# Performance work log

Hardware: AMD Instinct MI355X
Metric: run time of the kernel (lower is better)

## Reference

```python
import math
import jax, jax.numpy as jnp
import numpy as np

BLOCK = 32          # hard-coded in the CUDA kernels
NUM_HEADS = 16
NUM_BLOCKS = 512    # (max_pos//32) * block_per_row = 128 * 4
DIAG_N = 3
FIRST_N = 0


def _mra2_attention(Q, K, V, mask):
    # Q,K,V: (meta_batch, seq, head_dim); mask: (meta_batch, seq) in {0,1}
    mb, seq_len, d = Q.shape
    bs = BLOCK
    nb = seq_len // bs
    scale = 1.0 / math.sqrt(d)
    Q = Q * mask[:, :, None]
    K = K * mask[:, :, None]
    V = V * mask[:, :, None]

    # ---- low resolution block means (mask-weighted), approx_mode='full' keeps V_hat
    tc = mask.reshape(mb, nb, bs).sum(-1)                 # token count per block
    denom = tc[:, :, None] + 1e-6
    Q_hat = Q.reshape(mb, nb, bs, d).sum(2) / denom       # (mb, nb, d)
    K_hat = K.reshape(mb, nb, bs, d).sum(2) / denom
    V_hat = V.reshape(mb, nb, bs, d).sum(2) / denom
    low_logit = jnp.einsum('bid,bjd->bij', Q_hat, K_hat) * scale
    row_max = low_logit.max(-1, keepdims=True)            # before mask subtraction
    low_logit = low_logit - 10000.0 * ((tc[:, None, :] * tc[:, :, None]) < 0.5).astype(Q.dtype)

    # ---- block index selection (torch runs this under no_grad)
    lrn = jax.lax.stop_gradient(low_logit - row_max)
    if DIAG_N > 0:
        off = DIAG_N // 2
        i = jnp.arange(nb)
        band = (jnp.abs(i[:, None] - i[None, :]) <= off).astype(Q.dtype)
        lrn = lrn + band[None] * 5000.0
    if FIRST_N > 0:
        lrn = lrn.at[:, :FIRST_N, :].add(5000.0)
        lrn = lrn.at[:, :, :FIRST_N].add(5000.0)
    top_vals, indices = jax.lax.top_k(lrn.reshape(mb, nb * nb), NUM_BLOCKS)
    threshold = top_vals.min(-1)
    high_mask = (lrn >= threshold[:, None, None]).astype(Q.dtype)  # selected-block mask

    q_blk = indices // nb                                  # (mb, n) query block ids
    k_blk = indices % nb                                   # (mb, n) key block ids
    Qs = jnp.take_along_axis(Q.reshape(mb, nb, bs, d), q_blk[:, :, None, None], axis=1)
    Ks = jnp.take_along_axis(K.reshape(mb, nb, bs, d), k_blk[:, :, None, None], axis=1)
    Vs = jnp.take_along_axis(V.reshape(mb, nb, bs, d), k_blk[:, :, None, None], axis=1)

    # sampled dense-dense: sparse_C[b,n,k,q] (key-in-block, query-in-block layout as in kernel)
    hi_logit = jnp.einsum('bnkd,bnqd->bnkq', Ks, Qs) * scale

    # per query-row max over selected blocks (kernel index_max; constant for grad)
    b_idx = jnp.arange(mb)[:, None]
    blk_max = hi_logit.max(axis=2)                         # (mb, n, bs) max over key axis
    max_blocks = jnp.full((mb, nb, bs), -1e8, Q.dtype).at[b_idx, q_blk].max(blk_max)
    max_blocks = jax.lax.stop_gradient(max_blocks)
    max_vals = max_blocks.reshape(mb, seq_len)
    max_scatter = jnp.take_along_axis(max_blocks, q_blk[:, :, None], axis=1)[:, :, None, :]

    # key-side mask per selected block (sparse_mask_B)
    mask_blk = jnp.take_along_axis(mask.reshape(mb, nb, bs), k_blk[:, :, None], axis=1)
    hi_attn = jnp.exp(hi_logit - max_scatter - 10000.0 * (1.0 - mask_blk[:, :, :, None]))

    # sparse-dense matmul + reduce-sum normalizer, scattered back per query block
    hi_out = jnp.zeros((mb, nb, bs, d), Q.dtype).at[b_idx, q_blk].add(
        jnp.einsum('bnkq,bnkd->bnqd', hi_attn, Vs)).reshape(mb, seq_len, d)
    hi_norm = jnp.zeros((mb, nb, bs), Q.dtype).at[b_idx, q_blk].add(
        hi_attn.sum(axis=2)).reshape(mb, seq_len)

    # ---- low resolution branch, selected blocks suppressed via high_mask
    low_attn = jnp.exp(low_logit - row_max - 10000.0 * high_mask) * tc[:, None, :]
    low_out = jnp.repeat(jnp.einsum('bij,bjd->bid', low_attn, V_hat), bs, axis=1)
    low_norm = jnp.repeat(low_attn.sum(-1), bs, axis=1)

    log_corr = (jnp.repeat(row_max[:, :, 0], bs, axis=1) - max_vals) * mask
    low_corr = jnp.exp(jnp.minimum(log_corr, 0.0))
    hi_corr = jnp.exp(-jnp.maximum(log_corr, 0.0))

    ctx = hi_out * hi_corr[:, :, None] + low_out * low_corr[:, :, None]
    ctx = ctx / (hi_norm * hi_corr + low_norm * low_corr + 1e-6)[:, :, None]
    return ctx * mask[:, :, None]


def _forward(hidden_states, attention_mask, w_q, b_q, w_k, b_k, w_v, b_v):
    b, s, hdim = hidden_states.shape
    h = NUM_HEADS
    dh = hdim // h

    def split_heads(x):
        return x.reshape(b, s, h, dh).transpose(0, 2, 1, 3).reshape(b * h, s, dh)

    q = split_heads(hidden_states @ w_q.T + b_q)
    k = split_heads(hidden_states @ w_k.T + b_k)
    v = split_heads(hidden_states @ w_v.T + b_v)
    # invert extended additive mask (1 + am/10000) and replicate over heads
    # (torch's .repeat(1, h, 1).reshape(b*h, s) stacks h copies of the [b,s] mask)
    mask = jnp.tile(1.0 + attention_mask / 10000.0, (h, 1))
    ctx = _mra2_attention(q, k, v, mask)
    ctx = ctx.reshape(b, h, s, dh).transpose(0, 2, 1, 3).reshape(b, s, hdim)
    return ctx


def setup_inputs() -> dict:
    key = jax.random.key(0)
    ks = jax.random.split(key, 4)
    H = 1024
    return {
        'hidden_states': jax.random.normal(ks[0], (2, 4096, H), jnp.float32),
        'attention_mask': jnp.zeros((2, 4096), jnp.float32),
        'w_q': jax.random.normal(ks[1], (H, H), jnp.float32) * 0.02,
        'b_q': jnp.zeros((H,), jnp.float32),
        'w_k': jax.random.normal(ks[2], (H, H), jnp.float32) * 0.02,
        'b_k': jnp.zeros((H,), jnp.float32),
        'w_v': jax.random.normal(ks[3], (H, H), jnp.float32) * 0.02,
        'b_v': jnp.zeros((H,), jnp.float32),
    }


def reference(hidden_states, attention_mask, w_q, b_q, w_k, b_k, w_v, b_v):
    return _forward(hidden_states, attention_mask, w_q, b_q, w_k, b_k, w_v, b_v)
```

## Files before the change

kernel.cpp:

```cpp
#include <hip/hip_runtime.h>
#include <cstdint>
#include <cstddef>

#define MAXSEL 160
static constexpr int S    = 4096;
static constexpr int H    = 1024;
static constexpr int DH   = 64;
static constexpr int NB   = 128;
static constexpr int MBH  = 32;
static constexpr int M8   = 8192;
static constexpr int N3   = 3072;

typedef _Float16 half8 __attribute__((ext_vector_type(8)));
typedef _Float16 half4v __attribute__((ext_vector_type(4)));
typedef float floatx4 __attribute__((ext_vector_type(4)));

__device__ __forceinline__ void load_lds16(const void* g, void* l) {
  __builtin_amdgcn_global_load_lds((const __attribute__((address_space(1))) unsigned int*)g,
                                   (__attribute__((address_space(3))) unsigned int*)l,
                                   16, 0, 0);
}

__global__ __launch_bounds__(256) void k_prep(const float* __restrict__ hidden,
                                              const float* __restrict__ am,
                                              const float* __restrict__ wq,
                                              const float* __restrict__ wk,
                                              const float* __restrict__ wv,
                                              _Float16* __restrict__ h16,
                                              _Float16* __restrict__ w16,
                                              _Float16* __restrict__ wlo,
                                              _Float16* __restrict__ hb_hi,
                                              _Float16* __restrict__ hb_lo,
                                              float* __restrict__ tcv,
                                              int* __restrict__ selcnt) {
  const int blk_id = blockIdx.x;
  if (blk_id < 256) {
    if (blk_id == 0) {
      for (int i = threadIdx.x; i < MBH * NB; i += 256) selcnt[i] = 0;
    }
    int b2 = blk_id >> 7, blk = blk_id & 127;
    int c = threadIdx.x * 4;
    float4 s0 = make_float4(0.f, 0.f, 0.f, 0.f);
    float4 s1 = make_float4(0.f, 0.f, 0.f, 0.f);
    for (int i = 0; i < 32; i += 4) {
      int pos0 = blk * 32 + i;
      size_t base = ((size_t)b2 * 4096 + pos0) * 1024 + c;
      const float4 x0 = *(const float4*)&hidden[base];
      const float4 x1 = *(const float4*)&hidden[base + 1024];
      const float4 x2 = *(const float4*)&hidden[base + 2048];
      const float4 x3 = *(const float4*)&hidden[base + 3072];
      float a00 = am[pos0],      a01 = am[pos0 + 1],      a02 = am[pos0 + 2],      a03 = am[pos0 + 3];
      float a10 = am[4096+pos0], a11 = am[4096+pos0 + 1], a12 = am[4096+pos0 + 2], a13 = am[4096+pos0 + 3];
      half4v h;
      h[0]=(_Float16)x0.x; h[1]=(_Float16)x0.y; h[2]=(_Float16)x0.z; h[3]=(_Float16)x0.w;
      *(half4v*)&h16[base] = h;
      h[0]=(_Float16)x1.x; h[1]=(_Float16)x1.y; h[2]=(_Float16)x1.z; h[3]=(_Float16)x1.w;
      *(half4v*)&h16[base + 1024] = h;
      h[0]=(_Float16)x2.x; h[1]=(_Float16)x2.y; h[2]=(_Float16)x2.z; h[3]=(_Float16)x2.w;
      *(half4v*)&h16[base + 2048] = h;
      h[0]=(_Float16)x3.x; h[1]=(_Float16)x3.y; h[2]=(_Float16)x3.z; h[3]=(_Float16)x3.w;
      *(half4v*)&h16[base + 3072] = h;
      float m0, m1;
      m0 = 1.f + a00 * 1e-4f; m1 = 1.f + a10 * 1e-4f;
      s0.x += m0*x0.x; s0.y += m0*x0.y; s0.z += m0*x0.z; s0.w += m0*x0.w;
      s1.x += m1*x0.x; s1.y += m1*x0.y; s1.z += m1*x0.z; s1.w += m1*x0.w;
      m0 = 1.f + a01 * 1e-4f; m1 = 1.f + a11 * 1e-4f;
      s0.x += m0*x1.x; s0.y += m0*x1.y; s0.z += m0*x1.z; s0.w += m0*x1.w;
      s1.x += m1*x1.x; s1.y += m1*x1.y; s1.z += m1*x1.z; s1.w += m1*x1.w;
      m0 = 1.f + a02 * 1e-4f; m1 = 1.f + a12 * 1e-4f;
      s0.x += m0*x2.x; s0.y += m0*x2.y; s0.z += m0*x2.z; s0.w += m0*x2.w;
      s1.x += m1*x2.x; s1.y += m1*x2.y; s1.z += m1*x2.z; s1.w += m1*x2.w;
      m0 = 1.f + a03 * 1e-4f; m1 = 1.f + a13 * 1e-4f;
      s0.x += m0*x3.x; s0.y += m0*x3.y; s0.z += m0*x3.z; s0.w += m0*x3.w;
      s1.x += m1*x3.x; s1.y += m1*x3.y; s1.z += m1*x3.z; s1.w += m1*x3.w;
    }
    size_t row0 = (size_t)(b2 * 2 + 0) * 128 + blk;
    size_t row1 = (size_t)(b2 * 2 + 1) * 128 + blk;
    half4v hi, lo;
    hi[0]=(_Float16)s0.x; lo[0]=(_Float16)(s0.x-(float)hi[0]);
    hi[1]=(_Float16)s0.y; lo[1]=(_Float16)(s0.y-(float)hi[1]);
    hi[2]=(_Float16)s0.z; lo[2]=(_Float16)(s0.z-(float)hi[2]);
    hi[3]=(_Float16)s0.w; lo[3]=(_Float16)(s0.w-(float)hi[3]);
    *(half4v*)&hb_hi[row0 * 1024 + c] = hi;
    *(half4v*)&hb_lo[row0 * 1024 + c] = lo;
    hi[0]=(_Float16)s1.x; lo[0]=(_Float16)(s1.x-(float)hi[0]);
    hi[1]=(_Float16)s1.y; lo[1]=(_Float16)(s1.y-(float)hi[1]);
    hi[2]=(_Float16)s1.z; lo[2]=(_Float16)(s1.z-(float)hi[2]);
    hi[3]=(_Float16)s1.w; lo[3]=(_Float16)(s1.w-(float)hi[3]);
    *(half4v*)&hb_hi[row1 * 1024 + c] = hi;
    *(half4v*)&hb_lo[row1 * 1024 + c] = lo;
    if (b2 == 0 && threadIdx.x == 0) {
      float t0 = 0.f, t1 = 0.f;
      for (int i = 0; i < 32; ++i) {
        int pos = blk * 32 + i;
        t0 += 1.f + am[pos] * 1e-4f;
        t1 += 1.f + am[4096 + pos] * 1e-4f;
      }
      tcv[blk] = t0; tcv[128 + blk] = t1;
    }
  } else {
    long j = (long)(blk_id - 256) * 256 + threadIdx.x;
    const long NW4 = (long)H * H / 4;
    int which = (int)(j / NW4);
    long jj = j - (long)which * NW4;
    const float* src = which == 0 ? wq : (which == 1 ? wk : wv);
    float4 x = ((const float4*)src)[jj];
    half4v h;
    h[0] = (_Float16)x.x; h[1] = (_Float16)x.y;
    h[2] = (_Float16)x.z; h[3] = (_Float16)x.w;
    *(half4v*)&w16[j * 4] = h;
    if (which < 2) {
      half4v r;
      r[0] = (_Float16)(x.x - (float)h[0]);
      r[1] = (_Float16)(x.y - (float)h[1]);
      r[2] = (_Float16)(x.z - (float)h[2]);
      r[3] = (_Float16)(x.w - (float)h[3]);
      *(half4v*)&wlo[j * 4] = r;
    }
  }
}

__global__ __launch_bounds__(512, 4) void k_gemm_qkv(const _Float16* __restrict__ A,
                                                     const _Float16* __restrict__ B,
                                                     const float* __restrict__ bq,
                                                     const float* __restrict__ bk,
                                                     const float* __restrict__ bv,
                                                     const float* __restrict__ am,
                                                     _Float16* __restrict__ q16,
                                                     _Float16* __restrict__ k16,
                                                     _Float16* __restrict__ v16,
                                                     const _Float16* __restrict__ Ahi,
                                                     const _Float16* __restrict__ Alo,
                                                     const _Float16* __restrict__ Blo,
                                                     float* __restrict__ sideQK) {
  __shared__ _Float16 sh[36864];

  if (blockIdx.x < 768) {
    const int id = blockIdx.x;
    const int swz = (id & 7) * 96 + (id >> 3);
    const int by = swz / 12;
    const int bx = swz - by * 12;
    const int tid = threadIdx.x;
    const int lane = tid & 63, wv = tid >> 6;
    const int wm = wv >> 2, wn = wv & 3;
    const int l15 = lane & 15, quad = lane >> 4;

    _Float16* As = sh;
    _Float16* Bs = sh + 12288;

    floatx4 acc[4][4] = {};

    const _Float16* Ag = A + (size_t)(by * 128) * 1024;
    const _Float16* Bg = B + (size_t)(bx * 256) * 1024;

    const int gr  = lane >> 2;
    const int gcb = ((lane & 3) ^ ((lane >> 3) & 3)) * 8;
    const _Float16* agl  = Ag + (size_t)(wv * 16 + gr) * 1024 + gcb;
    const _Float16* bgl0 = Bg + (size_t)(wv * 32 + gr) * 1024 + gcb;
    const _Float16* bgl1 = Bg + (size_t)(wv * 32 + 16 + gr) * 1024 + gcb;
    const int aw  = (wv * 16) * 32;
    const int bw0 = (wv * 32) * 32;
    const int bw1 = (wv * 32 + 16) * 32;

#define STAGE(TT, BB)                                                   \
    {                                                                   \
      load_lds16(agl  + (size_t)(TT) * 32, &As[(BB) * 4096 + aw]);      \
      load_lds16(bgl0 + (size_t)(TT) * 32, &Bs[(BB) * 8192 + bw0]);     \
      load_lds16(bgl1 + (size_t)(TT) * 32, &Bs[(BB) * 8192 + bw1]);     \
    }

    STAGE(0, 0)
    STAGE(1, 1)

    const int rc = ((quad ^ ((l15 >> 1) & 3)) << 3);

#pragma unroll
    for (int t = 0; t < 32; ++t) {
      if (t == 31) { asm volatile("s_waitcnt vmcnt(0)" ::: "memory"); }
      else         { asm volatile("s_waitcnt vmcnt(3)" ::: "memory"); }
      __builtin_amdgcn_s_barrier();
      if (t < 30) {
        const int nb = (t + 2) % 3;
        STAGE(t + 2, nb)
      }
      const int bb = t % 3;
      half8 a[4], b[4];
#pragma unroll
      for (int mt = 0; mt < 4; ++mt)
        a[mt] = *(const half8*)&As[bb * 4096 + (wm * 64 + mt * 16 + l15) * 32 + rc];
#pragma unroll
      for (int nt = 0; nt < 4; ++nt)
        b[nt] = *(const half8*)&Bs[bb * 8192 + (wn * 64 + nt * 16 + l15) * 32 + rc];
      __builtin_amdgcn_s_setprio(1);
#pragma unroll
      for (int mt = 0; mt < 4; ++mt)
#pragma unroll
        for (int nt = 0; nt < 4; ++nt)
          acc[mt][nt] = __builtin_amdgcn_mfma_f32_16x16x32_f16(a[mt], b[nt], acc[mt][nt], 0, 0, 0);
      __builtin_amdgcn_s_setprio(0);
    }
#undef STAGE

    const int which = bx >> 2;
    const float* bias = which == 0 ? bq : (which == 1 ? bk : bv);
    _Float16* dst = which == 0 ? q16 : (which == 1 ? k16 : v16);
    const int hh = (bx & 3) * 4 + wn;
    const int m2 = hh & 1;
#pragma unroll
    for (int nt = 0; nt < 4; ++nt) {
      const int dd = nt * 16 + l15;
      const float bsv = bias[hh * 64 + dd];
#pragma unroll
      for (int mt = 0; mt < 4; ++mt) {
#pragma unroll
        for (int r = 0; r < 4; ++r) {
          int srow = by * 128 + wm * 64 + mt * 16 + quad * 4 + r;
          int b2 = srow >> 12, s = srow & 4095;
          float mv = 1.f + am[m2 * 4096 + s] * 1e-4f;
          float v = (acc[mt][nt][r] + bsv) * mv;
          int mb = b2 * 16 + hh;
          dst[((size_t)mb * 4096 + s) * 64 + dd] = (_Float16)v;
        }
      }
    }
    return;
  }

  const int half = threadIdx.x >> 8;
  const int stid = threadIdx.x & 255;
  const int sb   = (blockIdx.x - 768) * 2 + half;
  const int slane = stid & 63, swv = stid >> 6;
  const int kk  = sb >> 8;
  const int sbb = sb & 255;
  const int sbx = sbb & 31;
  const int sby = sbb >> 5;
  const int swm = swv >> 1, swn = swv & 1;
  const int sl15 = slane & 15, squad = slane >> 4;
  _Float16* base = sh + half * 16384;
  _Float16* sAhi = base;
  _Float16* sAlo = base + 4096;
  _Float16* sBhi = base + 8192;
  _Float16* sBlo = base + 12288;

  floatx4 acc[2][2] = {};

  const int srow = slane >> 3;
  const int scol = (((slane & 7) ^ (srow & 7)) * 8);
  const int sswz = sl15 & 7;
  const _Float16* src;
  _Float16* dst;
  if      (swv == 0) { src = Ahi + (size_t)(sby * 64) * 1024; dst = sAhi; }
  else if (swv == 1) { src = Alo + (size_t)(sby * 64) * 1024; dst = sAlo; }
  else if (swv == 2) { src = B   + (size_t)(sbx * 64) * 1024; dst = sBhi; }
  else               { src = Blo + (size_t)(sbx * 64) * 1024; dst = sBlo; }

  const int kbeg = kk * 512;
  for (int k0 = kbeg; k0 < kbeg + 512; k0 += 64) {
    __syncthreads();
#pragma unroll
    for (int i = 0; i < 8; ++i)
      load_lds16(src + (size_t)(i * 8 + srow) * 1024 + k0 + scol, dst + i * 512);
    __syncthreads();
#pragma unroll
    for (int ks = 0; ks < 2; ++ks) {
      const int kc = ks * 4;
      half8 ah[2], al[2], bh[2], bl[2];
#pragma unroll
      for (int mt = 0; mt < 2; ++mt) {
        int off = (swm * 32 + mt * 16 + sl15) * 64 + (((kc + squad) ^ sswz) << 3);
        ah[mt] = *(const half8*)&sAhi[off];
        al[mt] = *(const half8*)&sAlo[off];
      }
#pragma unroll
      for (int nt = 0; nt < 2; ++nt) {
        int off = (swn * 32 + nt * 16 + sl15) * 64 + (((kc + squad) ^ sswz) << 3);
        bh[nt] = *(const half8*)&sBhi[off];
        bl[nt] = *(const half8*)&sBlo[off];
      }
#pragma unroll
      for (int mt = 0; mt < 2; ++mt)
#pragma unroll
        for (int nt = 0; nt < 2; ++nt) {
          acc[mt][nt] = __builtin_amdgcn_mfma_f32_16x16x32_f16(ah[mt], bh[nt], acc[mt][nt], 0, 0, 0);
          acc[mt][nt] = __builtin_amdgcn_mfma_f32_16x16x32_f16(ah[mt], bl[nt], acc[mt][nt], 0, 0, 0);
          acc[mt][nt] = __builtin_amdgcn_mfma_f32_16x16x32_f16(al[mt], bh[nt], acc[mt][nt], 0, 0, 0);
        }
    }
  }
  float* outp = sideQK + (size_t)kk * (512 * 2048);
#pragma unroll
  for (int mt = 0; mt < 2; ++mt)
#pragma unroll
    for (int nt = 0; nt < 2; ++nt)
#pragma unroll
      for (int rr = 0; rr < 4; ++rr) {
        int row = sby * 64 + swm * 32 + mt * 16 + squad * 4 + rr;
        int col = sbx * 64 + swn * 32 + nt * 16 + sl15;
        outp[(size_t)row * 2048 + col] = acc[mt][nt][rr];
      }
}

__global__ __launch_bounds__(256) void k_lowlogit(const float* __restrict__ sideQK,
                                                  const float* __restrict__ tcv,
                                                  const float* __restrict__ bq,
                                                  const float* __restrict__ bk,
                                                  float* __restrict__ ll,
                                                  float* __restrict__ rmaxout,
                                                  const _Float16* __restrict__ v16,
                                                  float* __restrict__ vhat,
                                                  _Float16* __restrict__ v16T) {
  __shared__ __attribute__((aligned(16))) char shraw[37376];
  const int tid = threadIdx.x;

  if (blockIdx.x >= 256) {
    const int lane = tid & 63, wv = tid >> 6;
    _Float16* Vs = (_Float16*)shraw + wv * 2304;
    int bid = (blockIdx.x - 256) * 4 + wv;
    int mb = bid >> 7, blk = bid & 127;
    const _Float16* src = v16 + ((size_t)mb * 4096 + blk * 32) * 64;
    int r = lane >> 3, c = (lane & 7) * 8;
#pragma unroll
    for (int it = 0; it < 4; ++it)
      *(uint4*)&Vs[(it * 8 + r) * 72 + c] = *(const uint4*)&src[(it * 8 + r) * 64 + c];
    __syncthreads();
    float acc = 0.f;
    half8 col[4];
#pragma unroll
    for (int k = 0; k < 32; ++k) {
      _Float16 x = Vs[k * 72 + lane];
      col[k >> 3][k & 7] = x;
      acc += (float)x;
    }
    vhat[(size_t)bid * 64 + lane] = acc / (tcv[(mb & 1) * 128 + blk] + 1e-6f);
    _Float16* dst = v16T + (size_t)(mb * 64 + lane) * 4096 + blk * 32;
#pragma unroll
    for (int p = 0; p < 4; ++p) *(half8*)&dst[p * 8] = col[p];
    return;
  }

  const int mb = blockIdx.x >> 3;
  const int ib = blockIdx.x & 7;
  const int b2 = mb >> 4, m2 = mb & 1, hh = mb & 15;
  const int combo = b2 * 2 + m2;
  float* Kh  = (float*)shraw;
  float* Qh  = (float*)(shraw + 32768);
  float* tcL = (float*)(shraw + 32768 + 4096);

  const float* P1 = sideQK + (size_t)512 * 2048;

  if (tid < 128) tcL[tid] = tcv[m2 * 128 + tid];
  __syncthreads();
#pragma unroll
  for (int i = 0; i < 8; ++i) {
    int ci = tid + i * 256;
    int row = ci >> 4, c4 = (ci & 15) * 4;
    float tck = tcL[row];
    float den = 1.f / (tck + 1e-6f);
    size_t idx = ((size_t)combo * 128 + row) * 2048 + 1024 + hh * 64 + c4;
    float4 x0 = *(const float4*)&sideQK[idx];
    float4 x1 = *(const float4*)&P1[idx];
    float4 bb = *(const float4*)&bk[hh * 64 + c4];
    float4 o;
    o.x = (x0.x + x1.x + bb.x * tck) * den; o.y = (x0.y + x1.y + bb.y * tck) * den;
    o.z = (x0.z + x1.z + bb.z * tck) * den; o.w = (x0.w + x1.w + bb.w * tck) * den;
    *(float4*)&Kh[row * 64 + c4] = o;
  }
  {
    int row = tid >> 4, c4 = (tid & 15) * 4;
    int gi = ib * 16 + row;
    float tcq = tcL[gi];
    float den = 1.f / (tcq + 1e-6f);
    size_t idx = ((size_t)combo * 128 + gi) * 2048 + hh * 64 + c4;
    float4 x0 = *(const float4*)&sideQK[idx];
    float4 x1 = *(const float4*)&P1[idx];
    float4 bb = *(const float4*)&bq[hh * 64 + c4];
    float4 o;
    o.x = (x0.x + x1.x + bb.x * tcq) * den; o.y = (x0.y + x1.y + bb.y * tcq) * den;
    o.z = (x0.z + x1.z + bb.z * tcq) * den; o.w = (x0.w + x1.w + bb.w * tcq) * den;
    *(float4*)&Qh[row * 64 + c4] = o;
  }
  __syncthreads();

  const int il = tid >> 4, jg = tid & 15;
  const int i = ib * 16 + il;
  float tcq = tcL[i];
  float dots[8] = {};
#pragma unroll
  for (int dd = 0; dd < 16; ++dd) {
    int d4 = ((dd + tid) & 15) * 4;
    float4 qv = *(const float4*)&Qh[il * 64 + d4];
#pragma unroll
    for (int jj = 0; jj < 8; ++jj) {
      float4 kv = *(const float4*)&Kh[(jg * 8 + jj) * 64 + d4];
      dots[jj] += qv.x * kv.x + qv.y * kv.y + qv.z * kv.z + qv.w * kv.w;
    }
  }
  float tmax = -1e30f;
#pragma unroll
  for (int jj = 0; jj < 8; ++jj) {
    int j = jg * 8 + jj;
    float raw = dots[jj] * 0.125f;
    tmax = fmaxf(tmax, raw);
    float pen = (tcq * tcL[j] < 0.5f) ? 10000.f : 0.f;
    ll[(size_t)mb * 16384 + (size_t)i * 128 + j] = raw - pen;
  }
#pragma unroll
  for (int mk = 1; mk < 16; mk <<= 1) tmax = fmaxf(tmax, __shfl_xor(tmax, mk));
  if (jg == 0) rmaxout[mb * 128 + i] = tmax;
}

__global__ __launch_bounds__(256) void k_topk(const float* __restrict__ ll,
                                              const float* __restrict__ rmax,
                                              float* __restrict__ thr,
                                              int* __restrict__ selcnt,
                                              int* __restrict__ selkb) {
  const int mb = blockIdx.x;
  const int t = threadIdx.x;
  const int wid = t >> 6;
  __shared__ int red2[2][4];

  unsigned code[64];
#pragma unroll
  for (int j = 0; j < 64; ++j) {
    int e = j * 256 + t;
    int i = e >> 7, jj = e & 127;
    float lrn = ll[(size_t)mb * 16384 + e] - rmax[mb * 128 + i];
    int di = i - jj;
    if (di <= 1 && di >= -1) lrn += 5000.f;
    unsigned b = __float_as_uint(lrn);
    code[j] = (b & 0x80000000u) ? ~b : (b | 0x80000000u);
  }

  unsigned lo = 0u, hi = 0xFFFFFFFFu;
  for (int it = 0; it < 32; ++it) {
    unsigned mid = lo + ((hi - lo) >> 1);
    int c = 0;
#pragma unroll
    for (int j = 0; j < 64; ++j) c += (code[j] >= mid) ? 1 : 0;
#pragma unroll
    for (int mk = 1; mk < 64; mk <<= 1) c += __shfl_xor(c, mk);
    if ((t & 63) == 0) red2[it & 1][wid] = c;
    __syncthreads();
    int total = red2[it & 1][0] + red2[it & 1][1] + red2[it & 1][2] + red2[it & 1][3];
    if (total >= 512) lo = mid; else hi = mid;
  }
  if (t == 0) {
    unsigned bits = (lo & 0x80000000u) ? (lo & 0x7FFFFFFFu) : ~lo;
    thr[mb] = __uint_as_float(bits);
  }
#pragma unroll
  for (int j = 0; j < 64; ++j) {
    if (code[j] >= lo) {
      int e = j * 256 + t;
      int i = e >> 7, jj = e & 127;
      int slot = atomicAdd(&selcnt[mb * 128 + i], 1);
      if (slot < MAXSEL) selkb[(size_t)(mb * 128 + i) * MAXSEL + slot] = jj;
    }
  }
}

__global__ __launch_bounds__(64) void k_hi(const _Float16* __restrict__ q16,
                                           const _Float16* __restrict__ k16,
                                           const _Float16* __restrict__ v16T,
                                           const int* __restrict__ selcnt,
                                           const int* __restrict__ selkb,
                                           const float* __restrict__ rmax,
                                           const float* __restrict__ thr,
                                           const float* __restrict__ tcv,
                                           const float* __restrict__ vhat,
                                           const float* __restrict__ ll,
                                           const float* __restrict__ am,
                                           float* __restrict__ out) {
  const int mb = blockIdx.x & 31, qb = blockIdx.x >> 5;
  const int sid = mb * 128 + qb;
  const int lane = threadIdx.x;
  const int l15 = lane & 15, quad = lane >> 4;
  const int m2 = mb & 1, b2 = mb >> 4, hh = mb & 15;

  __shared__ _Float16 Ps[32 * 40];

  const _Float16* qbase = q16 + ((size_t)mb * 4096 + qb * 32) * 64;
  half8 aq[2][2];
#pragma unroll
  for (int mt = 0; mt < 2; ++mt)
#pragma unroll
    for (int ks = 0; ks < 2; ++ks)
      aq[mt][ks] = *(const half8*)&qbase[(mt * 16 + l15) * 64 + ks * 32 + quad * 8];

  const float rmaxb = rmax[sid];
  const float th = thr[mb];
  const float* llrow = ll + (size_t)mb * 16384 + (size_t)qb * 128;
  const float* tcrow = tcv + m2 * 128;
  const float* vhbase = vhat + ((size_t)(mb * 128)) * 64 + lane;
  float a0 = 0.f, a1 = 0.f, a2 = 0.f, a3 = 0.f;
  float n0 = 0.f, n1 = 0.f, n2 = 0.f, n3 = 0.f;
#pragma unroll 2
  for (int j0 = 0; j0 < 128; j0 += 4) {
    float4 l4 = *(const float4*)&llrow[j0];
    float4 t4 = *(const float4*)&tcrow[j0];
    float v0 = vhbase[(size_t)(j0 + 0) * 64];
    float v1 = vhbase[(size_t)(j0 + 1) * 64];
    float v2 = vhbase[(size_t)(j0 + 2) * 64];
    float v3 = vhbase[(size_t)(j0 + 3) * 64];
    int d0 = qb - j0;
    float lr0 = l4.x - rmaxb + ((d0 <= 1 && d0 >= -1) ? 5000.f : 0.f);
    float lr1 = l4.y - rmaxb + ((d0 <= 2 && d0 >= 0) ? 5000.f : 0.f);
    float lr2 = l4.z - rmaxb + ((d0 <= 3 && d0 >= 1) ? 5000.f : 0.f);
    float lr3 = l4.w - rmaxb + ((d0 <= 4 && d0 >= 2) ? 5000.f : 0.f);
    float w0 = (lr0 >= th) ? 0.f : __expf(l4.x - rmaxb) * t4.x;
    float w1 = (lr1 >= th) ? 0.f : __expf(l4.y - rmaxb) * t4.y;
    float w2 = (lr2 >= th) ? 0.f : __expf(l4.z - rmaxb) * t4.z;
    float w3 = (lr3 >= th) ? 0.f : __expf(l4.w - rmaxb) * t4.w;
    a0 += w0 * v0; a1 += w1 * v1; a2 += w2 * v2; a3 += w3 * v3;
    n0 += w0; n1 += w1; n2 += w2; n3 += w3;
  }
  float accL = (a0 + a1) + (a2 + a3);
  float nrmL = (n0 + n1) + (n2 + n3);

  int nk = selcnt[sid];
  if (nk > MAXSEL) nk = MAXSEL;
  const int* list = selkb + (size_t)sid * MAXSEL;

  const _Float16* kbase  = k16  + (size_t)mb * 4096 * 64;
  const _Float16* vtbase = v16T + (size_t)mb * 64 * 4096;

  float rm[2][4];
  floatx4 o[2][4] = {};
  floatx4 onrm[2] = {};
#pragma unroll
  for (int mt = 0; mt < 2; ++mt)
#pragma unroll
    for (int r = 0; r < 4; ++r) rm[mt][r] = -1e8f;

  half8 ones;
#pragma unroll
  for (int j = 0; j < 8; ++j) ones[j] = (_Float16)1.f;

  for (int t = 0; t < nk; ++t) {
    const int kb = list[t];
    const _Float16* kp = kbase + (size_t)kb * 32 * 64;
    half8 b0[2], b1[2];
#pragma unroll
    for (int ks = 0; ks < 2; ++ks) {
      b0[ks] = *(const half8*)&kp[(l15) * 64 + ks * 32 + quad * 8];
      b1[ks] = *(const half8*)&kp[(16 + l15) * 64 + ks * 32 + quad * 8];
    }
    const _Float16* vp = vtbase + kb * 32 + quad * 8;
    half8 vb0 = *(const half8*)&vp[(size_t)(l15) * 4096];
    half8 vb1 = *(const half8*)&vp[(size_t)(16 + l15) * 4096];
    half8 vb2 = *(const half8*)&vp[(size_t)(32 + l15) * 4096];
    half8 vb3 = *(const half8*)&vp[(size_t)(48 + l15) * 4096];

    floatx4 sf[2][2] = {};
    sf[0][0] = __builtin_amdgcn_mfma_f32_16x16x32_f16(aq[0][0], b0[0], sf[0][0], 0, 0, 0);
    sf[0][0] = __builtin_amdgcn_mfma_f32_16x16x32_f16(aq[0][1], b0[1], sf[0][0], 0, 0, 0);
    sf[0][1] = __builtin_amdgcn_mfma_f32_16x16x32_f16(aq[0][0], b1[0], sf[0][1], 0, 0, 0);
    sf[0][1] = __builtin_amdgcn_mfma_f32_16x16x32_f16(aq[0][1], b1[1], sf[0][1], 0, 0, 0);
    sf[1][0] = __builtin_amdgcn_mfma_f32_16x16x32_f16(aq[1][0], b0[0], sf[1][0], 0, 0, 0);
    sf[1][0] = __builtin_amdgcn_mfma_f32_16x16x32_f16(aq[1][1], b0[1], sf[1][0], 0, 0, 0);
    sf[1][1] = __builtin_amdgcn_mfma_f32_16x16x32_f16(aq[1][0], b1[0], sf[1][1], 0, 0, 0);
    sf[1][1] = __builtin_amdgcn_mfma_f32_16x16x32_f16(aq[1][1], b1[1], sf[1][1], 0, 0, 0);

    float pen0, pen1;
    {
      float mk0 = 1.f + am[m2 * 4096 + kb * 32 + l15] * 1e-4f;
      float mk1 = 1.f + am[m2 * 4096 + kb * 32 + 16 + l15] * 1e-4f;
      pen0 = 10000.f * (1.f - mk0);
      pen1 = 10000.f * (1.f - mk1);
    }
#pragma unroll
    for (int mt = 0; mt < 2; ++mt)
#pragma unroll
      for (int r = 0; r < 4; ++r) {
        float s0 = sf[mt][0][r] * 0.125f;
        float s1 = sf[mt][1][r] * 0.125f;
        float v = fmaxf(s0, s1);
#pragma unroll
        for (int mk = 1; mk < 16; mk <<= 1) v = fmaxf(v, __shfl_xor(v, mk));
        float mnew  = fmaxf(rm[mt][r], v);
        float alpha = __expf(rm[mt][r] - mnew);
        rm[mt][r] = mnew;
        float p0 = __expf(s0 - mnew - pen0);
        float p1 = __expf(s1 - mnew - pen1);
        o[mt][0][r] *= alpha; o[mt][1][r] *= alpha;
        o[mt][2][r] *= alpha; o[mt][3][r] *= alpha;
        onrm[mt][r] *= alpha;
        int row = mt * 16 + quad * 4 + r;
        Ps[row * 40 + l15] = (_Float16)p0;
        Ps[row * 40 + 16 + l15] = (_Float16)p1;
      }
    __syncthreads();
    half8 pa0 = *(const half8*)&Ps[(l15) * 40 + quad * 8];
    half8 pa1 = *(const half8*)&Ps[(16 + l15) * 40 + quad * 8];
    o[0][0] = __builtin_amdgcn_mfma_f32_16x16x32_f16(pa0, vb0, o[0][0], 0, 0, 0);
    o[0][1] = __builtin_amdgcn_mfma_f32_16x16x32_f16(pa0, vb1, o[0][1], 0, 0, 0);
    o[0][2] = __builtin_amdgcn_mfma_f32_16x16x32_f16(pa0, vb2, o[0][2], 0, 0, 0);
    o[0][3] = __builtin_amdgcn_mfma_f32_16x16x32_f16(pa0, vb3, o[0][3], 0, 0, 0);
    o[1][0] = __builtin_amdgcn_mfma_f32_16x16x32_f16(pa1, vb0, o[1][0], 0, 0, 0);
    o[1][1] = __builtin_amdgcn_mfma_f32_16x16x32_f16(pa1, vb1, o[1][1], 0, 0, 0);
    o[1][2] = __builtin_amdgcn_mfma_f32_16x16x32_f16(pa1, vb2, o[1][2], 0, 0, 0);
    o[1][3] = __builtin_amdgcn_mfma_f32_16x16x32_f16(pa1, vb3, o[1][3], 0, 0, 0);
    onrm[0] = __builtin_amdgcn_mfma_f32_16x16x32_f16(pa0, ones, onrm[0], 0, 0, 0);
    onrm[1] = __builtin_amdgcn_mfma_f32_16x16x32_f16(pa1, ones, onrm[1], 0, 0, 0);
    __syncthreads();
  }

  float lo_d[4];
#pragma unroll
  for (int ntd = 0; ntd < 4; ++ntd) lo_d[ntd] = __shfl(accL, ntd * 16 + l15);
#pragma unroll
  for (int mt = 0; mt < 2; ++mt) {
#pragma unroll
    for (int r = 0; r < 4; ++r) {
      int q = mt * 16 + quad * 4 + r;
      int qpos = qb * 32 + q;
      float mq = 1.f + am[m2 * 4096 + qpos] * 1e-4f;
      float logc = (rmaxb - rm[mt][r]) * mq;
      float lc = __expf(fminf(logc, 0.f));
      float hc = __expf(-fmaxf(logc, 0.f));
      float den = onrm[mt][r] * hc + nrmL * lc + 1e-6f;
      float sc = mq / den;
#pragma unroll
      for (int ntd = 0; ntd < 4; ++ntd) {
        float val = (o[mt][ntd][r] * hc + lo_d[ntd] * lc) * sc;
        out[((size_t)b2 * 4096 + qpos) * 1024 + hh * 64 + ntd * 16 + l15] = val;
      }
    }
  }
}

extern "C" void kernel_launch(void* const* d_in, const int* in_sizes, int n_in,
                              void* d_out, int out_size, void* d_ws, size_t ws_size,
                              hipStream_t stream) {
  const float* hidden = (const float*)d_in[0];
  const float* am     = (const float*)d_in[1];
  const float* wq     = (const float*)d_in[2];
  const float* bq     = (const float*)d_in[3];
  const float* wk     = (const float*)d_in[4];
  const float* bk     = (const float*)d_in[5];
  const float* wv     = (const float*)d_in[6];
  const float* bv     = (const float*)d_in[7];
  float* out = (float*)d_out;

  char* ws = (char*)d_ws;
  size_t off = 0;
  auto alloc = [&](size_t bytes) -> char* {
    char* p = ws + off;
    off += (bytes + 255) & ~(size_t)255;
    return p;
  };
  _Float16* h16    = (_Float16*)alloc((size_t)M8 * H * 2);
  _Float16* w16    = (_Float16*)alloc((size_t)N3 * H * 2);
  _Float16* wlo    = (_Float16*)alloc((size_t)2 * H * H * 2);
  _Float16* q16    = (_Float16*)alloc((size_t)MBH * S * DH * 2);
  _Float16* k16    = (_Float16*)alloc((size_t)MBH * S * DH * 2);
  _Float16* v16    = (_Float16*)alloc((size_t)MBH * S * DH * 2);
  _Float16* hb_hi  = (_Float16*)alloc((size_t)4 * NB * H * 2);
  _Float16* hb_lo  = (_Float16*)alloc((size_t)4 * NB * H * 2);
  float* tcv       = (float*)alloc((size_t)2 * NB * 4);
  float* sideQK    = (float*)alloc((size_t)2 * 512 * 2048 * 4);
  float* ll        = (float*)alloc((size_t)MBH * NB * NB * 4);
  float* rmax      = (float*)alloc((size_t)MBH * NB * 4);
  float* thr       = (float*)alloc((size_t)MBH * 4);
  int*   selcnt    = (int*)alloc((size_t)MBH * NB * 4);
  int*   selkb     = (int*)alloc((size_t)MBH * NB * MAXSEL * 4);
  float* vhat      = (float*)alloc((size_t)MBH * NB * DH * 4);
  _Float16* v16T   = h16;

  k_prep<<<dim3(3328), dim3(256), 0, stream>>>(hidden, am, wq, wk, wv,
                                               h16, w16, wlo, hb_hi, hb_lo, tcv, selcnt);
  k_gemm_qkv<<<dim3(1024), dim3(512), 0, stream>>>(h16, w16, bq, bk, bv, am,
                                                   q16, k16, v16,
                                                   hb_hi, hb_lo, wlo, sideQK);
  k_lowlogit<<<dim3(1280), dim3(256), 0, stream>>>(sideQK, tcv, bq, bk, ll, rmax,
                                                   v16, vhat, v16T);
  k_topk<<<dim3(32), dim3(256), 0, stream>>>(ll, rmax, thr, selcnt, selkb);
  k_hi<<<dim3(4096), dim3(64), 0, stream>>>(q16, k16, v16T, selcnt, selkb, rmax, thr,
                                            tcv, vhat, ll, am, out);
}
```

Measured before the change: 278.2 us.

## Block-tile transposed V layout, prefetch first key-block ids, drop barriers in sparse loop

The transposed V buffer is now stored per key block as contiguous 64x32 tiles, so each selected block's V fragment comes from one 4KB region instead of 64 rows strided by 4096. The first eight selected key-block indices are preloaded as two int4 vectors and picked with selects, which removes a dependent global load at the start of early iterations. The two __syncthreads around the P staging in shared memory are replaced by an LDS waitcnt with scheduling barriers. This relies on the attention kernel running as a single wavefront per block; with more waves the missing barrier would be a race.

After: 278.7 us, median of 2. Within noise of the previous version (+0.2%).

```diff
diff --git a/kernel.cpp b/kernel.cpp
--- a/kernel.cpp
+++ b/kernel.cpp
@@ -19,6 +19,18 @@
   __builtin_amdgcn_global_load_lds((const __attribute__((address_space(1))) unsigned int*)g,
                                    (__attribute__((address_space(3))) unsigned int*)l,
                                    16, 0, 0);
+}
+
+__device__ __forceinline__ int sel8(int t, int4 a, int4 b) {
+  int r = a.x;
+  r = (t == 1) ? a.y : r;
+  r = (t == 2) ? a.z : r;
+  r = (t == 3) ? a.w : r;
+  r = (t == 4) ? b.x : r;
+  r = (t == 5) ? b.y : r;
+  r = (t == 6) ? b.z : r;
+  r = (t == 7) ? b.w : r;
+  return r;
 }
 
 __global__ __launch_bounds__(256) void k_prep(const float* __restrict__ hidden,
@@ -332,7 +344,7 @@
       acc += (float)x;
     }
     vhat[(size_t)bid * 64 + lane] = acc / (tcv[(mb & 1) * 128 + blk] + 1e-6f);
-    _Float16* dst = v16T + (size_t)(mb * 64 + lane) * 4096 + blk * 32;
+    _Float16* dst = v16T + ((size_t)(mb * 128 + blk) * 64 + lane) * 32;
 #pragma unroll
     for (int p = 0; p < 4; ++p) *(half8*)&dst[p * 8] = col[p];
     return;
@@ -486,6 +498,10 @@
 #pragma unroll
     for (int ks = 0; ks < 2; ++ks)
       aq[mt][ks] = *(const half8*)&qbase[(mt * 16 + l15) * 64 + ks * 32 + quad * 8];
+
+  const int* list = selkb + (size_t)sid * MAXSEL;
+  const int4 La = *(const int4*)&list[0];
+  const int4 Lb = *(const int4*)&list[4];
 
   const float rmaxb = rmax[sid];
   const float th = thr[mb];
@@ -519,10 +535,9 @@
 
   int nk = selcnt[sid];
   if (nk > MAXSEL) nk = MAXSEL;
-  const int* list = selkb + (size_t)sid * MAXSEL;
 
   const _Float16* kbase  = k16  + (size_t)mb * 4096 * 64;
-  const _Float16* vtbase = v16T + (size_t)mb * 64 * 4096;
+  const _Float16* vtbase = v16T + (size_t)mb * 128 * 2048;
 
   float rm[2][4];
   floatx4 o[2][4] = {};
@@ -537,7 +552,7 @@
   for (int j = 0; j < 8; ++j) ones[j] = (_Float16)1.f;
 
   for (int t = 0; t < nk; ++t) {
-    const int kb = list[t];
+    const int kb = (t < 8) ? sel8(t, La, Lb) : list[t];
     const _Float16* kp = kbase + (size_t)kb * 32 * 64;
     half8 b0[2], b1[2];
 #pragma unroll
@@ -545,11 +560,11 @@
       b0[ks] = *(const half8*)&kp[(l15) * 64 + ks * 32 + quad * 8];
       b1[ks] = *(const half8*)&kp[(16 + l15) * 64 + ks * 32 + quad * 8];
     }
-    const _Float16* vp = vtbase + kb * 32 + quad * 8;
-    half8 vb0 = *(const half8*)&vp[(size_t)(l15) * 4096];
-    half8 vb1 = *(const half8*)&vp[(size_t)(16 + l15) * 4096];
-    half8 vb2 = *(const half8*)&vp[(size_t)(32 + l15) * 4096];
-    half8 vb3 = *(const half8*)&vp[(size_t)(48 + l15) * 4096];
+    const _Float16* vp = vtbase + kb * 2048 + quad * 8;
+    half8 vb0 = *(const half8*)&vp[(l15) * 32];
+    half8 vb1 = *(const half8*)&vp[(16 + l15) * 32];
+    half8 vb2 = *(const half8*)&vp[(32 + l15) * 32];
+    half8 vb3 = *(const half8*)&vp[(48 + l15) * 32];
 
     floatx4 sf[2][2] = {};
     sf[0][0] = __builtin_amdgcn_mfma_f32_16x16x32_f16(aq[0][0], b0[0], sf[0][0], 0, 0, 0);
@@ -589,7 +604,9 @@
         Ps[row * 40 + l15] = (_Float16)p0;
         Ps[row * 40 + 16 + l15] = (_Float16)p1;
       }
-    __syncthreads();
+    __builtin_amdgcn_sched_barrier(0);
+    asm volatile("s_waitcnt lgkmcnt(0)" ::: "memory");
+    __builtin_amdgcn_sched_barrier(0);
     half8 pa0 = *(const half8*)&Ps[(l15) * 40 + quad * 8];
     half8 pa1 = *(const half8*)&Ps[(16 + l15) * 40 + quad * 8];
     o[0][0] = __builtin_amdgcn_mfma_f32_16x16x32_f16(pa0, vb0, o[0][0], 0, 0, 0);
@@ -602,7 +619,6 @@
     o[1][3] = __builtin_amdgcn_mfma_f32_16x16x32_f16(pa1, vb3, o[1][3], 0, 0, 0);
     onrm[0] = __builtin_amdgcn_mfma_f32_16x16x32_f16(pa0, ones, onrm[0], 0, 0, 0);
     onrm[1] = __builtin_amdgcn_mfma_f32_16x16x32_f16(pa1, ones, onrm[1], 0, 0, 0);
-    __syncthreads();
   }
 
   float lo_d[4];
```
